# Kernel optimization log

Measured on AMD Instinct MI355X. Metric: run time of the kernel, lower is better.

Reference implementation:

```python
import jax, jax.numpy as jnp
import numpy as np

B, T, M = 65536, 512, 12  # series, timesteps, seasonal period


def setup_inputs() -> dict:
    key = jax.random.key(0)
    kx, = jax.random.split(key, 1)
    x = jax.random.uniform(kx, (B, T, 1), dtype=jnp.float32) + 0.5  # positive series values
    init_alpha = 0.5 / M
    alpha = jnp.full((1, 1), init_alpha, dtype=jnp.float32)
    beta = jnp.full((1, 1), 0.1 * init_alpha, dtype=jnp.float32)
    phi = jnp.full((1, 1), 0.99, dtype=jnp.float32)
    gamma = jnp.full((1, 1), 0.5, dtype=jnp.float32)
    l0 = jnp.ones((B, 1), dtype=jnp.float32)
    b0 = jnp.zeros((B, 1), dtype=jnp.float32)
    s0 = jnp.ones((B, M), dtype=jnp.float32)
    return {"x": x, "alpha": alpha, "beta": beta, "phi": phi,
            "gamma": gamma, "l0": l0, "b0": b0, "s0": s0}


def reference(x, alpha, beta, phi, gamma, l0, b0, s0):
    # Holt-Winters ESRNN cell: additive trend, multiplicative season, period M.
    # Per step (matching the seasonal+trend branch of the Keras cell):
    #   l = a*(x/s0[:, :1]) + (1-a)*(l0 + b0*phi)
    #   b = be*(l - l0) + (1-be)*(b0*phi)
    #   s_new = g*(x/(l + b*phi)) + (1-g)*s0[:, :1]
    #   s = concat(s0[:,1:], s_new)
    #   out = (l + b*phi) * s0[:, 1:2]
    def step(carry, x_t):
        l_p, b_p, s_p = carry              # (B,1), (B,1), (B,M)
        lb_p = l_p + b_p * phi             # damped trend forecast of level
        l = alpha * (x_t / s_p[:, :1]) + (1.0 - alpha) * lb_p
        b = beta * (l - l_p) + (1.0 - beta) * (b_p * phi)
        s_new = gamma * (x_t / (l + b * phi)) + (1.0 - gamma) * s_p[:, :1]
        s = jnp.concatenate([s_p[:, 1:], s_new], axis=1)
        out = (l + b * phi) * s_p[:, 1:2]
        return (l, b, s), out

    x_tm = jnp.transpose(x, (1, 0, 2))     # (T,B,1) time-major for scan
    _, outs = jax.lax.scan(step, (l0, b0, s0), x_tm)
    return jnp.transpose(outs, (1, 0, 2))  # (B,T,1)
```

## Files before the change

kernel.cpp:

```cpp
#include <hip/hip_runtime.h>


constexpr int TT     = 512;
constexpr int TC     = 48;
constexpr int NCH    = 10;
constexpr int SW     = 64;
constexpr int SROW   = 64;
constexpr int PITCH4 = TT / 4;

typedef float f32x4 __attribute__((ext_vector_type(4)));

#define CBAR() asm volatile("" ::: "memory")

#define STEPM(XV, SH, SN, OV)                                              \
    do {                                                                   \
        const float s_h_ = ring[SH];                                       \
        const float q_   = (XV) * __builtin_amdgcn_rcpf(s_h_);             \
        const float lb_  = fmaf(b, phi, l);                                \
        const float ln_  = fmaf(alpha, q_, omal * lb_);                    \
        const float bphi_ = b * phi;                                       \
        const float bn_  = fmaf(beta, ln_ - l, ombe * bphi_);              \
        const float lb2_ = fmaf(bn_, phi, ln_);                            \
        const float sn_  = fmaf(gamma, (XV) * __builtin_amdgcn_rcpf(lb2_), \
                                omg * s_h_);                               \
        (OV) = lb2_ * ring[SN];                                            \
        ring[SH] = sn_;                                                    \
        l = ln_; b = bn_;                                                  \
    } while (0)

__global__ __launch_bounds__(64) void esrnn_kernel(
    const float* __restrict__ x,
    const float* __restrict__ p_alpha,
    const float* __restrict__ p_beta,
    const float* __restrict__ p_phi,
    const float* __restrict__ p_gamma,
    const float* __restrict__ l0,
    const float* __restrict__ b0,
    const float* __restrict__ s0,
    float* __restrict__ out)
{
    const int tid = threadIdx.x;
    const int t7  = tid & 7;
    const int series0 = blockIdx.x * SW;
    const int i = series0 + tid;

    __shared__ __align__(16) float lds_x[SW * SROW];
    __shared__ __align__(16) float lds_o[SW * SROW];

    const float alpha = p_alpha[0];
    const float beta  = p_beta[0];
    const float phi   = p_phi[0];
    const float gamma = p_gamma[0];
    const float omal  = 1.0f - alpha;
    const float ombe  = 1.0f - beta;
    const float omg   = 1.0f - gamma;

    float l = l0[i];
    float b = b0[i];

    float ring[12];
    {
        const f32x4* s04 = reinterpret_cast<const f32x4*>(s0 + (size_t)i * 12);
        f32x4 sa = s04[0], sb = s04[1], sc = s04[2];
        ring[0] = sa.x; ring[1] = sa.y; ring[2]  = sa.z; ring[3]  = sa.w;
        ring[4] = sb.x; ring[5] = sb.y; ring[6]  = sb.z; ring[7]  = sb.w;
        ring[8] = sc.x; ring[9] = sc.y; ring[10] = sc.z; ring[11] = sc.w;
    }

    int rr[12], qq[12], lo[12];
    #pragma unroll
    for (int m = 0; m < 12; ++m) {
        const int f = tid + SW * m;
        rr[m] = f / 12;
        qq[m] = f - 12 * rr[m];
        lo[m] = rr[m] * SROW + ((qq[m] ^ (rr[m] & 7)) << 2);
    }
    int rt[8], qt[8], lt[8];
    #pragma unroll
    for (int m = 0; m < 8; ++m) {
        const int f = tid + SW * m;
        rt[m] = f >> 3;
        qt[m] = f & 7;
        lt[m] = rt[m] * SROW + ((qt[m] ^ (rt[m] & 7)) << 2);
    }

    const f32x4* x4 = reinterpret_cast<const f32x4*>(x) + (size_t)series0 * PITCH4;
    f32x4*       o4 = reinterpret_cast<f32x4*>(out)     + (size_t)series0 * PITCH4;

    f32x4 vx[12], vn[12], vm[12];

    #pragma unroll
    for (int m = 0; m < 12; ++m)
        vx[m] = x4[(size_t)rr[m] * PITCH4 + qq[m]];
    #pragma unroll
    for (int m = 0; m < 12; ++m)
        vn[m] = x4[(size_t)rr[m] * PITCH4 + 12 + qq[m]];

    #pragma unroll 1
    for (int k = 0; k < NCH; ++k) {
        #pragma unroll
        for (int m = 0; m < 12; ++m)
            *reinterpret_cast<f32x4*>(&lds_x[lo[m]]) = vx[m];
        CBAR();

        if (k < NCH - 2) {
            #pragma unroll
            for (int m = 0; m < 12; ++m)
                vm[m] = x4[(size_t)rr[m] * PITCH4 + (k + 2) * 12 + qq[m]];
        } else if (k == NCH - 2) {
            #pragma unroll
            for (int m = 0; m < 8; ++m)
                vm[m] = x4[(size_t)rt[m] * PITCH4 + 120 + qt[m]];
        }
        CBAR();

        #pragma unroll
        for (int q = 0; q < 12; ++q) {
            const int sl = tid * SROW + ((q ^ t7) << 2);
            const f32x4 xq = *reinterpret_cast<const f32x4*>(&lds_x[sl]);
            f32x4 oq;
            STEPM(xq.x, (4 * q + 0) % 12, (4 * q + 1) % 12, oq.x);
            STEPM(xq.y, (4 * q + 1) % 12, (4 * q + 2) % 12, oq.y);
            STEPM(xq.z, (4 * q + 2) % 12, (4 * q + 3) % 12, oq.z);
            STEPM(xq.w, (4 * q + 3) % 12, (4 * q + 4) % 12, oq.w);
            *reinterpret_cast<f32x4*>(&lds_o[sl]) = oq;
        }
        CBAR();

        #pragma unroll
        for (int m = 0; m < 12; ++m) {
            const f32x4 o = *reinterpret_cast<const f32x4*>(&lds_o[lo[m]]);
            o4[(size_t)rr[m] * PITCH4 + k * 12 + qq[m]] = o;
        }
        CBAR();

        #pragma unroll
        for (int m = 0; m < 12; ++m) { vx[m] = vn[m]; vn[m] = vm[m]; }
    }

    {
        #pragma unroll
        for (int m = 0; m < 8; ++m)
            *reinterpret_cast<f32x4*>(&lds_x[lt[m]]) = vx[m];
        CBAR();
        #pragma unroll
        for (int q = 0; q < 8; ++q) {
            const int sl = tid * SROW + ((q ^ t7) << 2);
            const f32x4 xq = *reinterpret_cast<const f32x4*>(&lds_x[sl]);
            f32x4 oq;
            STEPM(xq.x, (4 * q + 0) % 12, (4 * q + 1) % 12, oq.x);
            STEPM(xq.y, (4 * q + 1) % 12, (4 * q + 2) % 12, oq.y);
            STEPM(xq.z, (4 * q + 2) % 12, (4 * q + 3) % 12, oq.z);
            STEPM(xq.w, (4 * q + 3) % 12, (4 * q + 4) % 12, oq.w);
            *reinterpret_cast<f32x4*>(&lds_o[sl]) = oq;
        }
        CBAR();
        #pragma unroll
        for (int m = 0; m < 8; ++m) {
            const f32x4 o = *reinterpret_cast<const f32x4*>(&lds_o[lt[m]]);
            o4[(size_t)rt[m] * PITCH4 + 120 + qt[m]] = o;
        }
    }
}

extern "C" void kernel_launch(void* const* d_in, const int* in_sizes, int n_in,
                              void* d_out, int out_size, void* d_ws, size_t ws_size,
                              hipStream_t stream)
{
    const float* x       = (const float*)d_in[0];
    const float* p_alpha = (const float*)d_in[1];
    const float* p_beta  = (const float*)d_in[2];
    const float* p_phi   = (const float*)d_in[3];
    const float* p_gamma = (const float*)d_in[4];
    const float* l0      = (const float*)d_in[5];
    const float* b0      = (const float*)d_in[6];
    const float* s0      = (const float*)d_in[7];
    float* out = (float*)d_out;

    const int B = in_sizes[5];
    const int grid = B / SW;

    esrnn_kernel<<<grid, SW, 0, stream>>>(x, p_alpha, p_beta, p_phi, p_gamma,
                                          l0, b0, s0, out);
}
```

Before: 57.59 us.

## Load inputs per-thread directly, drop LDS input transpose, use nontemporal output stores

Each thread now reads its own series row straight from global memory with 16-byte vector loads, so the LDS staging and transpose of the input is removed. That drops the LDS writes and reads for x and the shared buffer that held it. The output still goes through the LDS transpose, but the global writes are now nontemporal stores, and the global offsets are precomputed. The cost is that the x loads are strided across lanes (one 2 KB row per thread), so each wave touches many cache lines per load instruction instead of issuing coalesced loads.

```diff
diff --git a/kernel.cpp b/kernel.cpp
--- a/kernel.cpp
+++ b/kernel.cpp
@@ -44,7 +44,6 @@
     const int series0 = blockIdx.x * SW;
     const int i = series0 + tid;
 
-    __shared__ __align__(16) float lds_x[SW * SROW];
     __shared__ __align__(16) float lds_o[SW * SROW];
 
     const float alpha = p_alpha[0];
@@ -67,70 +66,64 @@
         ring[8] = sc.x; ring[9] = sc.y; ring[10] = sc.z; ring[11] = sc.w;
     }
 
-    int rr[12], qq[12], lo[12];
+    int gxo[12], lo[12];
     #pragma unroll
     for (int m = 0; m < 12; ++m) {
         const int f = tid + SW * m;
-        rr[m] = f / 12;
-        qq[m] = f - 12 * rr[m];
-        lo[m] = rr[m] * SROW + ((qq[m] ^ (rr[m] & 7)) << 2);
+        const int r = f / 12;
+        const int q = f - 12 * r;
+        gxo[m] = r * PITCH4 + q;
+        lo[m]  = r * SROW + ((q ^ (r & 7)) << 2);
     }
-    int rt[8], qt[8], lt[8];
+    int gxT[8], lt[8];
     #pragma unroll
     for (int m = 0; m < 8; ++m) {
         const int f = tid + SW * m;
-        rt[m] = f >> 3;
-        qt[m] = f & 7;
-        lt[m] = rt[m] * SROW + ((qt[m] ^ (rt[m] & 7)) << 2);
+        const int r = f >> 3;
+        const int q = f & 7;
+        gxT[m] = r * PITCH4 + 120 + q;
+        lt[m]  = r * SROW + ((q ^ (r & 7)) << 2);
     }
 
-    const f32x4* x4 = reinterpret_cast<const f32x4*>(x) + (size_t)series0 * PITCH4;
+    const f32x4* xr = reinterpret_cast<const f32x4*>(x) + (size_t)i * PITCH4;
     f32x4*       o4 = reinterpret_cast<f32x4*>(out)     + (size_t)series0 * PITCH4;
 
     f32x4 vx[12], vn[12], vm[12];
 
     #pragma unroll
-    for (int m = 0; m < 12; ++m)
-        vx[m] = x4[(size_t)rr[m] * PITCH4 + qq[m]];
+    for (int m = 0; m < 12; ++m) vx[m] = xr[m];
     #pragma unroll
-    for (int m = 0; m < 12; ++m)
-        vn[m] = x4[(size_t)rr[m] * PITCH4 + 12 + qq[m]];
+    for (int m = 0; m < 12; ++m) vn[m] = xr[12 + m];
 
     #pragma unroll 1
     for (int k = 0; k < NCH; ++k) {
-        #pragma unroll
-        for (int m = 0; m < 12; ++m)
-            *reinterpret_cast<f32x4*>(&lds_x[lo[m]]) = vx[m];
-        CBAR();
-
         if (k < NCH - 2) {
             #pragma unroll
             for (int m = 0; m < 12; ++m)
-                vm[m] = x4[(size_t)rr[m] * PITCH4 + (k + 2) * 12 + qq[m]];
+                vm[m] = xr[(k + 2) * 12 + m];
         } else if (k == NCH - 2) {
             #pragma unroll
             for (int m = 0; m < 8; ++m)
-                vm[m] = x4[(size_t)rt[m] * PITCH4 + 120 + qt[m]];
+                vm[m] = xr[120 + m];
         }
         CBAR();
 
         #pragma unroll
         for (int q = 0; q < 12; ++q) {
-            const int sl = tid * SROW + ((q ^ t7) << 2);
-            const f32x4 xq = *reinterpret_cast<const f32x4*>(&lds_x[sl]);
+            const f32x4 xq = vx[q];
             f32x4 oq;
             STEPM(xq.x, (4 * q + 0) % 12, (4 * q + 1) % 12, oq.x);
             STEPM(xq.y, (4 * q + 1) % 12, (4 * q + 2) % 12, oq.y);
             STEPM(xq.z, (4 * q + 2) % 12, (4 * q + 3) % 12, oq.z);
             STEPM(xq.w, (4 * q + 3) % 12, (4 * q + 4) % 12, oq.w);
-            *reinterpret_cast<f32x4*>(&lds_o[sl]) = oq;
+            *reinterpret_cast<f32x4*>(&lds_o[tid * SROW + ((q ^ t7) << 2)]) = oq;
         }
         CBAR();
 
         #pragma unroll
         for (int m = 0; m < 12; ++m) {
             const f32x4 o = *reinterpret_cast<const f32x4*>(&lds_o[lo[m]]);
-            o4[(size_t)rr[m] * PITCH4 + k * 12 + qq[m]] = o;
+            __builtin_nontemporal_store(o, &o4[gxo[m] + k * 12]);
         }
         CBAR();
 
@@ -140,25 +133,20 @@
 
     {
         #pragma unroll
-        for (int m = 0; m < 8; ++m)
-            *reinterpret_cast<f32x4*>(&lds_x[lt[m]]) = vx[m];
-        CBAR();
-        #pragma unroll
         for (int q = 0; q < 8; ++q) {
-            const int sl = tid * SROW + ((q ^ t7) << 2);
-            const f32x4 xq = *reinterpret_cast<const f32x4*>(&lds_x[sl]);
+            const f32x4 xq = vx[q];
             f32x4 oq;
             STEPM(xq.x, (4 * q + 0) % 12, (4 * q + 1) % 12, oq.x);
             STEPM(xq.y, (4 * q + 1) % 12, (4 * q + 2) % 12, oq.y);
             STEPM(xq.z, (4 * q + 2) % 12, (4 * q + 3) % 12, oq.z);
             STEPM(xq.w, (4 * q + 3) % 12, (4 * q + 4) % 12, oq.w);
-            *reinterpret_cast<f32x4*>(&lds_o[sl]) = oq;
+            *reinterpret_cast<f32x4*>(&lds_o[tid * SROW + ((q ^ t7) << 2)]) = oq;
         }
         CBAR();
         #pragma unroll
         for (int m = 0; m < 8; ++m) {
             const f32x4 o = *reinterpret_cast<const f32x4*>(&lds_o[lt[m]]);
-            o4[(size_t)rt[m] * PITCH4 + 120 + qt[m]] = o;
+            __builtin_nontemporal_store(o, &o4[gxT[m]]);
         }
     }
 }
```

Result: faster. 47.07 us (-18.3%).
